# Performance work log

Measured on AMD Instinct MI355X. Metric: run time of the kernel, lower is better.

Reference implementation:

```python
import jax, jax.numpy as jnp
import numpy as np

L, D, V = 3, 512, 100        # num_layers, num_dimensions, vocabulary_size
B, S, SE = 128, 512, 512     # batch, decoder seq len, encoder seq len


def setup_inputs() -> dict:
    key = jax.random.key(0)
    ks = jax.random.split(key, 16)
    s = 1.0 / np.sqrt(D)
    u = lambda k, shape: jax.random.uniform(k, shape, jnp.float32, -s, s)
    return {
        "padded_seqs": jax.random.randint(ks[0], (B, S), 0, V),
        "seq_lengths": jax.random.randint(ks[1], (B,), 1, S + 1),
        "encoder_padded_seqs": jax.random.normal(ks[2], (B, SE, D), jnp.float32),
        "hidden_states": jax.random.normal(ks[3], (L, B, D), jnp.float32),
        "embedding": jax.random.normal(ks[4], (V, D), jnp.float32) * 0.02,
        "gru_w_ih": u(ks[5], (L, 3 * D, D)),
        "gru_w_hh": u(ks[6], (L, 3 * D, D)),
        "gru_b_ih": u(ks[7], (L, 3 * D)),
        "gru_b_hh": u(ks[8], (L, 3 * D)),
        "attn_w": u(ks[9], (D, 2 * D)),
        "attn_b": u(ks[10], (D,)),
        "out_w": u(ks[11], (V, D)),
        "out_b": u(ks[12], (V,)),
    }


def _gru(x, h0, w_ih, w_hh, b_ih, b_hh):
    """Multi-layer GRU, batch_first. x:(B,S,D), h0:(L,B,D). PyTorch gate order r,z,n."""
    h_finals = []
    for l in range(L):
        # precompute input projections for all timesteps: (B,S,3D)
        xp = jnp.einsum('bsd,ed->bse', x, w_ih[l]) + b_ih[l]
        whh, bhh = w_hh[l], b_hh[l]

        def step(h, xt):
            gh = h @ whh.T + bhh                      # (B,3D)
            xr, xz, xn = jnp.split(xt, 3, axis=-1)
            hr, hz, hn = jnp.split(gh, 3, axis=-1)
            r = jax.nn.sigmoid(xr + hr)
            z = jax.nn.sigmoid(xz + hz)
            n = jnp.tanh(xn + r * hn)
            h2 = (1.0 - z) * n + z * h
            return h2, h2

        hT, ys = jax.lax.scan(step, h0[l], jnp.swapaxes(xp, 0, 1))
        x = jnp.swapaxes(ys, 0, 1)                    # (B,S,D) output of this layer
        h_finals.append(hT)
    return x, jnp.stack(h_finals)


def reference(padded_seqs, seq_lengths, encoder_padded_seqs, hidden_states,
              embedding, gru_w_ih, gru_w_hh, gru_b_ih, gru_b_hh,
              attn_w, attn_b, out_w, out_b):
    # embedding (dropout=0 in eval)
    emb = embedding[padded_seqs]                      # (B,S,D)
    dec, h_out = _gru(emb, hidden_states, gru_w_ih, gru_w_hh, gru_b_ih, gru_b_hh)
    # mask from first hidden channel, exactly as the torch code
    mask = (dec[:, :, 0] != 0).astype(jnp.float32)[:, :, None]   # (B,S,1)
    # attention: scaled dot-product scores over encoder positions
    scores = jnp.einsum('bqd,bkd->bqk', dec, encoder_padded_seqs) / np.sqrt(D)
    attn_w8 = jax.nn.softmax(scores, axis=2)          # (B,S,SE)
    context = jnp.einsum('bqk,bkd->bqd', attn_w8, encoder_padded_seqs)
    cat = jnp.concatenate([dec, context], axis=2)     # (B,S,2D)
    attn_masked = jnp.tanh(cat @ attn_w.T + attn_b) * mask
    logits = (attn_masked @ out_w.T + out_b) * mask   # (B,S,V)
    return logits, h_out, attn_w8
```

## Files before the change

kernel.cpp:

```cpp
#include <hip/hip_runtime.h>


typedef unsigned short u16;
typedef __attribute__((ext_vector_type(8))) __bf16 bf16x8;
typedef __attribute__((ext_vector_type(4))) float f32x4;
typedef __attribute__((ext_vector_type(4))) unsigned int u32x4;

#define D_ 512
#define S_ 512
#define SE_ 512
#define B_ 128
#define V_ 100

__device__ __forceinline__ float bf2f(u16 v) {
  unsigned u = ((unsigned)v) << 16;
  return __builtin_bit_cast(float, u);
}
__device__ __forceinline__ u16 f2bf(float f) {
  unsigned u = __builtin_bit_cast(unsigned, f);
  u += 0x7FFF + ((u >> 16) & 1);
  return (u16)(u >> 16);
}

__global__ __launch_bounds__(256) void cvt_f32_bf16(const float* __restrict__ src,
                                                    u16* __restrict__ dst, long n4) {
  long i = (long)blockIdx.x * 256 + threadIdx.x;
  long stride = (long)gridDim.x * 256;
  for (; i < n4; i += stride) {
    float4 v = ((const float4*)src)[i];
    unsigned long long p = (unsigned long long)f2bf(v.x) |
                           ((unsigned long long)f2bf(v.y) << 16) |
                           ((unsigned long long)f2bf(v.z) << 32) |
                           ((unsigned long long)f2bf(v.w) << 48);
    ((unsigned long long*)dst)[i] = p;
  }
}

__global__ __launch_bounds__(256) void zero_flags(unsigned* __restrict__ f, int n) {
  int i = blockIdx.x * 256 + threadIdx.x;
  if (i < n)
    __hip_atomic_store(&f[i], 0u, __ATOMIC_RELAXED, __HIP_MEMORY_SCOPE_AGENT);
}

__global__ __launch_bounds__(256) void transpose_enc(const float* __restrict__ enc,
                                                     u16* __restrict__ encT) {
  __shared__ u16 tile[64][72];
  int b = blockIdx.z, d0 = blockIdx.x * 64, se0 = blockIdx.y * 64;
  const float* src = enc + (long)b * SE_ * D_;
  int t = threadIdx.x;
  int r = t >> 2, cq = (t & 3) * 16;
#pragma unroll
  for (int j = 0; j < 4; ++j) {
    float4 v = *(const float4*)(src + (long)(se0 + r) * D_ + d0 + cq + j * 4);
    tile[r][cq + j * 4 + 0] = f2bf(v.x);
    tile[r][cq + j * 4 + 1] = f2bf(v.y);
    tile[r][cq + j * 4 + 2] = f2bf(v.z);
    tile[r][cq + j * 4 + 3] = f2bf(v.w);
  }
  __syncthreads();
  u16* dst = encT + (long)b * D_ * SE_;
  u16 ov[16];
#pragma unroll
  for (int j = 0; j < 16; ++j) ov[j] = tile[cq + j][r];
  *(u32x4*)(dst + (long)(d0 + r) * SE_ + se0 + cq) = *(u32x4*)&ov[0];
  *(u32x4*)(dst + (long)(d0 + r) * SE_ + se0 + cq + 8) = *(u32x4*)&ov[8];
}

__global__ __launch_bounds__(256) void softmax_rows(float* __restrict__ sc,
                                                    u16* __restrict__ abf) {
  long row = (long)blockIdx.x * 4 + (threadIdx.x >> 6);
  int lane = threadIdx.x & 63;
  float* p = sc + row * 512;
  float4 v0 = ((const float4*)p)[lane * 2];
  float4 v1 = ((const float4*)p)[lane * 2 + 1];
  float vals[8] = {v0.x, v0.y, v0.z, v0.w, v1.x, v1.y, v1.z, v1.w};
  float m = vals[0];
#pragma unroll
  for (int j = 1; j < 8; ++j) m = fmaxf(m, vals[j]);
#pragma unroll
  for (int o = 32; o; o >>= 1) m = fmaxf(m, __shfl_xor(m, o, 64));
  float s = 0.f;
#pragma unroll
  for (int j = 0; j < 8; ++j) { vals[j] = __expf(vals[j] - m); s += vals[j]; }
#pragma unroll
  for (int o = 32; o; o >>= 1) s += __shfl_xor(s, o, 64);
  float inv = 1.f / s;
  u16 ob[8];
#pragma unroll
  for (int j = 0; j < 8; ++j) { vals[j] *= inv; ob[j] = f2bf(vals[j]); }
  float4 w0 = {vals[0], vals[1], vals[2], vals[3]};
  float4 w1 = {vals[4], vals[5], vals[6], vals[7]};
  ((float4*)p)[lane * 2] = w0;
  ((float4*)p)[lane * 2 + 1] = w1;
  *(u32x4*)(abf + row * 512 + lane * 8) = *(u32x4*)ob;
}

template <int MODE, int WF32>
__global__ __launch_bounds__(256) void gemm_xwt(
    const u16* __restrict__ A1, const u16* __restrict__ A2, const u16* __restrict__ W,
    const float* __restrict__ bias, void* __restrict__ Cout, const u16* __restrict__ maskSrc,
    int N, int K, int K1, long sAb, long sWb, long sCb, float scale, int ldc) {
  __shared__ u16 sA[128][32];
  __shared__ u16 sW_[128][32];
  int bz = blockIdx.z;
  int n0 = blockIdx.x * 128, m0 = blockIdx.y * 128;
  const u16* Ab = A1 + (long)bz * sAb;
  int t = threadIdx.x, wave = t >> 6, lane = t & 63;
  int wm = (wave >> 1) * 64, wn = (wave & 1) * 64;
  f32x4 acc[4][4] = {};
  for (int kk = 0; kk < K; kk += 32) {
#pragma unroll
    for (int i = 0; i < 2; ++i) {
      int id = t + i * 256;
      int row = id >> 2, c8 = (id & 3) * 8;
      const u16* src;
      if (MODE == 3 && kk >= K1)
        src = A2 + (long)(m0 + row) * (K - K1) + (kk - K1) + c8;
      else
        src = Ab + (long)(m0 + row) * K1 + kk + c8;
      *(u32x4*)&sA[row][c8] = *(const u32x4*)src;
    }
#pragma unroll
    for (int i = 0; i < 2; ++i) {
      int id = t + i * 256;
      int row = id >> 2, c8 = (id & 3) * 8;
      if (WF32) {
        const float* wsrc = ((const float*)W) + (long)bz * sWb + (long)(n0 + row) * K + kk + c8;
        float4 va = *(const float4*)wsrc;
        float4 vb = *(const float4*)(wsrc + 4);
        u16 tmp[8] = {f2bf(va.x), f2bf(va.y), f2bf(va.z), f2bf(va.w),
                      f2bf(vb.x), f2bf(vb.y), f2bf(vb.z), f2bf(vb.w)};
        *(u32x4*)&sW_[row][c8] = *(u32x4*)tmp;
      } else {
        u32x4 v = {0u, 0u, 0u, 0u};
        if (n0 + row < N) v = *(const u32x4*)(W + (long)bz * sWb + (long)(n0 + row) * K + kk + c8);
        *(u32x4*)&sW_[row][c8] = v;
      }
    }
    __syncthreads();
    int k8 = (lane >> 4) * 8, rr = lane & 15;
    bf16x8 wf[4];
#pragma unroll
    for (int nt = 0; nt < 4; ++nt)
      wf[nt] = __builtin_bit_cast(bf16x8, *(const u32x4*)&sW_[wn + nt * 16 + rr][k8]);
#pragma unroll
    for (int mt = 0; mt < 4; ++mt) {
      bf16x8 af = __builtin_bit_cast(bf16x8, *(const u32x4*)&sA[wm + mt * 16 + rr][k8]);
#pragma unroll
      for (int nt = 0; nt < 4; ++nt)
        acc[mt][nt] = __builtin_amdgcn_mfma_f32_16x16x32_bf16(af, wf[nt], acc[mt][nt], 0, 0, 0);
    }
    __syncthreads();
  }
  int rq = (lane >> 4) * 4, cl = lane & 15;
#pragma unroll
  for (int mt = 0; mt < 4; ++mt) {
#pragma unroll
    for (int nt = 0; nt < 4; ++nt) {
#pragma unroll
      for (int rg = 0; rg < 4; ++rg) {
        int row = m0 + wm + mt * 16 + rq + rg;
        int col = n0 + wn + nt * 16 + cl;
        float v = acc[mt][nt][rg];
        if (MODE == 1) {
          ((float*)Cout)[(long)bz * sCb + (long)row * ldc + col] = v * scale;
        } else if (MODE == 2) {
          ((u16*)Cout)[(long)bz * sCb + (long)row * ldc + col] = f2bf(v);
        } else if (MODE == 3) {
          float mk = (bf2f(maskSrc[(long)row * D_]) != 0.f) ? 1.f : 0.f;
          ((u16*)Cout)[(long)row * ldc + col] = f2bf(tanhf(v + bias[col]) * mk);
        } else {
          if (col < N) {
            float mk = (bf2f(maskSrc[(long)row * D_]) != 0.f) ? 1.f : 0.f;
            ((float*)Cout)[(long)row * ldc + col] = (v + bias[col]) * mk;
          }
        }
      }
    }
  }
}

__global__ __launch_bounds__(512, 1) void gru_wave(
    const int* __restrict__ tok, const float* __restrict__ embedding,
    const u16* __restrict__ wih_all, const u16* __restrict__ whh_all,
    const float* __restrict__ bih_all, const float* __restrict__ bhh_all,
    const float* __restrict__ hidden,
    unsigned* __restrict__ ring01, unsigned* __restrict__ ring2,
    unsigned* __restrict__ ringM1, unsigned* __restrict__ flags,
    u16* __restrict__ xout2, float* __restrict__ hfin) {
  __shared__ u16 sHA[32 * 512];
  __shared__ u16 sHB[32 * 512];
  __shared__ float sXP[2][32 * 101];
  __shared__ float sPART[24 * 272];
  const int bid = blockIdx.x;
  const int l = bid >> 6;
  const int bg = (bid >> 4) & 3;
  const int cg = bid & 15;
  const int tid = threadIdx.x;
  const int wave = tid >> 6;
  const bool isXp = wave >= 4;
  const int nh = (wave >> 1) & 1;
  const int kh = wave & 1;
  const int lane = tid & 63;
  const int rr = lane & 15, kq = lane >> 4;
  const int cl = rr, rq = kq;
  const int chL = nh * 16 + cl;
  const int ch = cg * 32 + chL;
  unsigned* myflags = flags + (l * 4 + bg) * 32 * 16;
  const unsigned* belowflags = (l > 0) ? flags + ((l - 1) * 4 + bg) * 32 * 16 : myflags;
  const u16* Wsrc = (isXp ? wih_all : whh_all) + (long)l * 786432;
  const float* bsrc = (isXp ? bih_all : bhh_all) + l * 1536;
  float bh[3];
#pragma unroll
  for (int g = 0; g < 3; ++g) bh[g] = bsrc[g * 512 + ch];

  auto ringAddr = [&](int lay, int t) -> unsigned* {
    if (t < 0) return ringM1 + lay * 32768;
    if (lay == 2) return ring2 + (long)t * 32768;
    return ring01 + ((long)lay * 512 + t) * 32768;
  };

  u32x4 wf[3][8];
#pragma unroll
  for (int g = 0; g < 3; ++g) {
    const u16* wrow =
        Wsrc + ((long)(g * 512 + cg * 32 + nh * 16 + rr)) * 512 + kh * 256 + kq * 8;
#pragma unroll
    for (int ks = 0; ks < 8; ++ks) wf[g][ks] = *(const u32x4*)(wrow + ks * 32);
  }

  float mh[2][4] = {};
  if (!isXp && kh == 0) {
#pragma unroll
    for (int mt = 0; mt < 2; ++mt)
#pragma unroll
      for (int rg = 0; rg < 4; ++rg)
        mh[mt][rg] =
            hidden[(long)l * 65536 + (long)(bg * 32 + mt * 16 + rq * 4 + rg) * 512 + ch];
  }

#pragma unroll 1
  for (int t = -1; t < S_; ++t) {
    const bool doXp = isXp && (t < S_ - 1);
#pragma unroll
    for (int g = 0; g < 3; ++g)
#pragma unroll
      for (int ks = 0; ks < 8; ++ks) asm volatile("" : "+v"(wf[g][ks]));

    if (doXp && l == 0) {
      int u = tid - 256;
#pragma unroll
      for (int i = 0; i < 2; ++i) {
        int task = u + i * 256;
        int row = task >> 4;
        int c0 = (task & 15) * 32;
        int tk = tok[(long)(bg * 32 + row) * 512 + (t + 1)];
        const float* es = embedding + (long)tk * 512 + c0;
        u16 tmp[32];
#pragma unroll
        for (int q = 0; q < 8; ++q) {
          float4 v = *(const float4*)(es + q * 4);
          tmp[q * 4 + 0] = f2bf(v.x); tmp[q * 4 + 1] = f2bf(v.y);
          tmp[q * 4 + 2] = f2bf(v.z); tmp[q * 4 + 3] = f2bf(v.w);
        }
#pragma unroll
        for (int q = 0; q < 4; ++q) {
          int grp = (c0 >> 3) + q;
          *(u32x4*)&sHB[row * 512 + ((grp ^ (row & 7)) * 8)] = *(u32x4*)&tmp[q * 8];
        }
      }
    }
    asm volatile("" ::: "memory");
    if (wave == 0) {
      const unsigned* fp = nullptr;
      int tgt = 0;
      if (lane < 32) { fp = myflags + lane * 16; tgt = t + 1; }
      else if (l > 0 && t < S_ - 1) { fp = belowflags + (lane - 32) * 16; tgt = t + 3; }
      int it = 0;
      bool ok;
      do {
        int v = fp ? (int)__hip_atomic_load(fp, __ATOMIC_RELAXED, __HIP_MEMORY_SCOPE_AGENT)
                   : 0x3fffffff;
        ok = (bool)__all(v >= tgt);
        if (!ok) __builtin_amdgcn_s_sleep(1);
      } while (!ok && ++it < (1 << 22));
    }
    __syncthreads();
    if (!isXp && t >= 0) {
      const unsigned* hsrc = ringAddr(l, t - 1) + bg * 32 * 256;
      u32x4 vv[8];
#pragma unroll
      for (int i = 0; i < 8; ++i) {
        int uu = tid + i * 256;
        const unsigned* src = hsrc + (uu >> 6) * 256 + (uu & 63) * 4;
        asm volatile("global_load_dwordx4 %0, %1, off sc0 sc1"
                     : "=&v"(vv[i]) : "v"(src) : "memory");
      }
      asm volatile("s_waitcnt vmcnt(0)" ::: "memory");
      __builtin_amdgcn_sched_barrier(0);
#pragma unroll
      for (int i = 0; i < 8; ++i) {
        int uu = tid + i * 256;
        int row = uu >> 6, c8 = uu & 63;
        *(u32x4*)&sHA[row * 512 + ((c8 ^ (row & 7)) * 8)] = vv[i];
      }
    } else if (doXp && l > 0) {
      const unsigned* hsrc = ringAddr(l - 1, t + 1) + bg * 32 * 256;
      u32x4 vv[8];
#pragma unroll
      for (int i = 0; i < 8; ++i) {
        int uu = (tid - 256) + i * 256;
        const unsigned* src = hsrc + (uu >> 6) * 256 + (uu & 63) * 4;
        asm volatile("global_load_dwordx4 %0, %1, off sc0 sc1"
                     : "=&v"(vv[i]) : "v"(src) : "memory");
      }
      asm volatile("s_waitcnt vmcnt(0)" ::: "memory");
      __builtin_amdgcn_sched_barrier(0);
#pragma unroll
      for (int i = 0; i < 8; ++i) {
        int uu = (tid - 256) + i * 256;
        int row = uu >> 6, c8 = uu & 63;
        *(u32x4*)&sHB[row * 512 + ((c8 ^ (row & 7)) * 8)] = vv[i];
      }
    }
    __syncthreads();
    f32x4 acc[2][3] = {};
    const bool doMM = isXp ? doXp : (t >= 0);
    if (doMM) {
      const u16* sH = isXp ? sHB : sHA;
#pragma unroll
      for (int mt = 0; mt < 2; ++mt) {
        const int abase = (mt * 16 + rr) * 512;
        const int axor = (mt * 16 + rr) & 7;
#pragma unroll
        for (int ks = 0; ks < 8; ++ks) {
          const int grp = kh * 32 + ks * 4 + kq;
          bf16x8 af = __builtin_bit_cast(
              bf16x8, *(const u32x4*)&sH[abase + ((grp ^ axor) * 8)]);
#pragma unroll
          for (int g = 0; g < 3; ++g)
            acc[mt][g] = __builtin_amdgcn_mfma_f32_16x16x32_bf16(
                af, __builtin_bit_cast(bf16x8, wf[g][ks]), acc[mt][g], 0, 0, 0);
        }
      }
      if (kh == 1) {
#pragma unroll
        for (int mt = 0; mt < 2; ++mt)
#pragma unroll
          for (int g = 0; g < 3; ++g) {
            float* sp = &sPART[((((isXp ? 2 : 0) + nh) * 2 + mt) * 3 + g) * 272];
#pragma unroll
            for (int rg = 0; rg < 4; ++rg)
              sp[(rq * 4 + rg) * 17 + cl] = acc[mt][g][rg];
          }
      }
    }
    __syncthreads();
    if (doMM && kh == 0) {
#pragma unroll
      for (int mt = 0; mt < 2; ++mt)
#pragma unroll
        for (int g = 0; g < 3; ++g) {
          const float* sp = &sPART[((((isXp ? 2 : 0) + nh) * 2 + mt) * 3 + g) * 272];
#pragma unroll
          for (int rg = 0; rg < 4; ++rg)
            acc[mt][g][rg] += sp[(rq * 4 + rg) * 17 + cl];
        }
      if (isXp) {
        float* xpd = sXP[(t + 1) & 1];
#pragma unroll
        for (int mt = 0; mt < 2; ++mt)
#pragma unroll
          for (int g = 0; g < 3; ++g)
#pragma unroll
            for (int rg = 0; rg < 4; ++rg)
              xpd[(mt * 16 + rq * 4 + rg) * 101 + g * 32 + chL] =
                  acc[mt][g][rg] + bh[g];
      }
    }
    if (!isXp && kh == 0) {
      const float* xps = sXP[t & 1];
      unsigned* rdst = ringAddr(l, t);
      unsigned xsv[2][4];
#pragma unroll
      for (int mt = 0; mt < 2; ++mt) {
        unsigned pk[4];
#pragma unroll
        for (int rg = 0; rg < 4; ++rg) {
          float h2;
          if (t >= 0) {
            int rloc = mt * 16 + rq * 4 + rg;
            float xr = xps[rloc * 101 + chL];
            float xz = xps[rloc * 101 + 32 + chL];
            float xn = xps[rloc * 101 + 64 + chL];
            float r = 1.f / (1.f + __expf(-(xr + acc[mt][0][rg] + bh[0])));
            float z = 1.f / (1.f + __expf(-(xz + acc[mt][1][rg] + bh[1])));
            float n = tanhf(xn + r * (acc[mt][2][rg] + bh[2]));
            h2 = (1.f - z) * n + z * mh[mt][rg];
            mh[mt][rg] = h2;
          } else {
            h2 = mh[mt][rg];
          }
          pk[rg] = (unsigned)f2bf(h2);
        }
        xsv[mt][0] = pk[0]; xsv[mt][1] = pk[1]; xsv[mt][2] = pk[2]; xsv[mt][3] = pk[3];
#pragma unroll
        for (int rg = 0; rg < 4; ++rg) {
          unsigned prt = (unsigned)__shfl_xor((int)pk[rg], 1);
          if (!(cl & 1))
            __hip_atomic_store(
                &rdst[(bg * 32 + mt * 16 + rq * 4 + rg) * 256 + (ch >> 1)],
                pk[rg] | (prt << 16), __ATOMIC_RELAXED, __HIP_MEMORY_SCOPE_AGENT);
        }
      }
      asm volatile("s_waitcnt vmcnt(0)" ::: "memory");
      if (lane == 0)
        __hip_atomic_store(&myflags[(cg * 2 + nh) * 16], (unsigned)(t + 2),
                           __ATOMIC_RELAXED, __HIP_MEMORY_SCOPE_AGENT);
      if (l == 2 && t >= 0) {
#pragma unroll
        for (int mt = 0; mt < 2; ++mt)
#pragma unroll
          for (int rg = 0; rg < 4; ++rg) {
            int rloc = mt * 16 + rq * 4 + rg;
            xout2[((long)(bg * 32 + rloc) * 512 + t) * 512 + ch] = (u16)xsv[mt][rg];
          }
      }
    }
  }
  if (!isXp && kh == 0) {
#pragma unroll
    for (int mt = 0; mt < 2; ++mt)
#pragma unroll
      for (int rg = 0; rg < 4; ++rg)
        hfin[(long)l * 65536 + (long)(bg * 32 + mt * 16 + rq * 4 + rg) * 512 + ch] =
            mh[mt][rg];
  }
}

extern "C" void kernel_launch(void* const* d_in, const int* in_sizes, int n_in,
                              void* d_out, int out_size, void* d_ws, size_t ws_size,
                              hipStream_t stream) {
  const int* padded    = (const int*)d_in[0];
  const float* enc     = (const float*)d_in[2];
  const float* hidden  = (const float*)d_in[3];
  const float* embedding = (const float*)d_in[4];
  const float* w_ih    = (const float*)d_in[5];
  const float* w_hh    = (const float*)d_in[6];
  const float* b_ih    = (const float*)d_in[7];
  const float* b_hh    = (const float*)d_in[8];
  const float* attn_w  = (const float*)d_in[9];
  const float* attn_b  = (const float*)d_in[10];
  const float* out_w   = (const float*)d_in[11];
  const float* out_b   = (const float*)d_in[12];

  if (ws_size < 280645632ULL) return;

  char* ws = (char*)d_ws;
  u16* W_IH   = (u16*)(ws + 0);
  u16* W_HH   = (u16*)(ws + 4718592);
  u16* ATTN_W = (u16*)(ws + 9437184);
  u16* OUT_W  = (u16*)(ws + 10485760);
  unsigned* FLAGS = (unsigned*)(ws + 10588160);
  unsigned* RINGM1 = (unsigned*)(ws + 10637312);
  u16* XA     = (u16*)(ws + 12210176);
  u16* XB     = (u16*)(ws + 79319040);
  u16* ENCT   = (u16*)(ws + 146427904);
  u16* AMASK  = (u16*)(ws + 213536768);
  u16* ATTN_BF = AMASK;

  float* out_logits = (float*)d_out;
  float* out_h      = out_logits + 6553600;
  float* out_attn   = out_h + 196608;

  unsigned* RING01 = (unsigned*)out_attn;
  unsigned* RING2  = (unsigned*)XA;

  zero_flags<<<24, 256, 0, stream>>>(FLAGS, 6144);
  cvt_f32_bf16<<<512, 256, 0, stream>>>(w_ih, W_IH, 2359296 / 4);
  cvt_f32_bf16<<<512, 256, 0, stream>>>(w_hh, W_HH, 2359296 / 4);
  cvt_f32_bf16<<<256, 256, 0, stream>>>(attn_w, ATTN_W, 524288 / 4);
  cvt_f32_bf16<<<64, 256, 0, stream>>>(out_w, OUT_W, 51200 / 4);
  transpose_enc<<<dim3(8, 8, 128), 256, 0, stream>>>(enc, ENCT);

  gru_wave<<<192, 512, 0, stream>>>(
      padded, embedding, W_IH, W_HH, b_ih, b_hh, hidden,
      RING01, RING2, RINGM1, FLAGS, XB, out_h);

  gemm_xwt<1, 1><<<dim3(4, 4, 128), 256, 0, stream>>>(
      XB, nullptr, (const u16*)enc, nullptr, out_attn, nullptr,
      512, 512, 512, 262144, 262144, 262144, 0.044194173824159216f, 512);
  softmax_rows<<<16384, 256, 0, stream>>>(out_attn, ATTN_BF);
  gemm_xwt<2, 0><<<dim3(4, 4, 128), 256, 0, stream>>>(
      ATTN_BF, nullptr, ENCT, nullptr, XA, nullptr,
      512, 512, 512, 262144, 262144, 262144, 1.f, 512);
  gemm_xwt<3, 0><<<dim3(4, 512, 1), 256, 0, stream>>>(
      XB, XA, ATTN_W, attn_b, AMASK, XB,
      512, 1024, 512, 0, 0, 0, 1.f, 512);
  gemm_xwt<4, 0><<<dim3(1, 512, 1), 256, 0, stream>>>(
      AMASK, nullptr, OUT_W, out_b, d_out, XB,
      100, 512, 512, 0, 0, 0, 1.f, 100);
}
```

Baseline: 3.340 ms.

## Deepen GRU input-projection pipeline to two steps ahead with triple-buffered sXP

The persistent wavefront GRU kernel now computes the input projection two timesteps ahead of the recurrent step instead of one. It uses a three-slot sXP buffer and shifts the flag targets and ring indices to match. The aim is more slack between layers, so a layer's x-projection for a future step does not wait on the layer below producing its output. The cost is one extra warm-up iteration, more shared memory, and a deeper wait on the below-layer flags. That deeper wait could lengthen the cross-layer critical path.

```diff
diff --git a/kernel.cpp b/kernel.cpp
--- a/kernel.cpp
+++ b/kernel.cpp
@@ -190,7 +190,7 @@
     u16* __restrict__ xout2, float* __restrict__ hfin) {
   __shared__ u16 sHA[32 * 512];
   __shared__ u16 sHB[32 * 512];
-  __shared__ float sXP[2][32 * 101];
+  __shared__ float sXP[3][32 * 101];
   __shared__ float sPART[24 * 272];
   const int bid = blockIdx.x;
   const int l = bid >> 6;
@@ -240,8 +240,9 @@
   }
 
 #pragma unroll 1
-  for (int t = -1; t < S_; ++t) {
-    const bool doXp = isXp && (t < S_ - 1);
+  for (int p = -2; p < S_; ++p) {
+    const bool doXp = isXp && (p <= S_ - 3);
+    const bool doGh = !isXp && (p >= 0);
 #pragma unroll
     for (int g = 0; g < 3; ++g)
 #pragma unroll
@@ -254,7 +255,7 @@
         int task = u + i * 256;
         int row = task >> 4;
         int c0 = (task & 15) * 32;
-        int tk = tok[(long)(bg * 32 + row) * 512 + (t + 1)];
+        int tk = tok[(long)(bg * 32 + row) * 512 + (p + 2)];
         const float* es = embedding + (long)tk * 512 + c0;
         u16 tmp[32];
 #pragma unroll
@@ -274,8 +275,8 @@
     if (wave == 0) {
       const unsigned* fp = nullptr;
       int tgt = 0;
-      if (lane < 32) { fp = myflags + lane * 16; tgt = t + 1; }
-      else if (l > 0 && t < S_ - 1) { fp = belowflags + (lane - 32) * 16; tgt = t + 3; }
+      if (lane < 32 && p >= 0) { fp = myflags + lane * 16; tgt = p + 2; }
+      else if (lane >= 32 && l > 0 && p <= S_ - 3) { fp = belowflags + (lane - 32) * 16; tgt = p + 5; }
       int it = 0;
       bool ok;
       do {
@@ -286,8 +287,8 @@
       } while (!ok && ++it < (1 << 22));
     }
     __syncthreads();
-    if (!isXp && t >= 0) {
-      const unsigned* hsrc = ringAddr(l, t - 1) + bg * 32 * 256;
+    if (doGh) {
+      const unsigned* hsrc = ringAddr(l, p - 1) + bg * 32 * 256;
       u32x4 vv[8];
 #pragma unroll
       for (int i = 0; i < 8; ++i) {
@@ -305,7 +306,7 @@
         *(u32x4*)&sHA[row * 512 + ((c8 ^ (row & 7)) * 8)] = vv[i];
       }
     } else if (doXp && l > 0) {
-      const unsigned* hsrc = ringAddr(l - 1, t + 1) + bg * 32 * 256;
+      const unsigned* hsrc = ringAddr(l - 1, p + 2) + bg * 32 * 256;
       u32x4 vv[8];
 #pragma unroll
       for (int i = 0; i < 8; ++i) {
@@ -325,7 +326,7 @@
     }
     __syncthreads();
     f32x4 acc[2][3] = {};
-    const bool doMM = isXp ? doXp : (t >= 0);
+    const bool doMM = isXp ? doXp : doGh;
     if (doMM) {
       const u16* sH = isXp ? sHB : sHA;
 #pragma unroll
@@ -367,7 +368,7 @@
             acc[mt][g][rg] += sp[(rq * 4 + rg) * 17 + cl];
         }
       if (isXp) {
-        float* xpd = sXP[(t + 1) & 1];
+        float* xpd = sXP[(p + 2) % 3];
 #pragma unroll
         for (int mt = 0; mt < 2; ++mt)
 #pragma unroll
@@ -378,9 +379,9 @@
                   acc[mt][g][rg] + bh[g];
       }
     }
-    if (!isXp && kh == 0) {
-      const float* xps = sXP[t & 1];
-      unsigned* rdst = ringAddr(l, t);
+    if (!isXp && kh == 0 && p >= -1) {
+      const float* xps = sXP[((p % 3) + 3) % 3];
+      unsigned* rdst = ringAddr(l, p);
       unsigned xsv[2][4];
 #pragma unroll
       for (int mt = 0; mt < 2; ++mt) {
@@ -388,7 +389,7 @@
 #pragma unroll
         for (int rg = 0; rg < 4; ++rg) {
           float h2;
-          if (t >= 0) {
+          if (p >= 0) {
             int rloc = mt * 16 + rq * 4 + rg;
             float xr = xps[rloc * 101 + chL];
             float xz = xps[rloc * 101 + 32 + chL];
@@ -415,15 +416,15 @@
       }
       asm volatile("s_waitcnt vmcnt(0)" ::: "memory");
       if (lane == 0)
-        __hip_atomic_store(&myflags[(cg * 2 + nh) * 16], (unsigned)(t + 2),
+        __hip_atomic_store(&myflags[(cg * 2 + nh) * 16], (unsigned)(p + 3),
                            __ATOMIC_RELAXED, __HIP_MEMORY_SCOPE_AGENT);
-      if (l == 2 && t >= 0) {
+      if (l == 2 && p >= 0) {
 #pragma unroll
         for (int mt = 0; mt < 2; ++mt)
 #pragma unroll
           for (int rg = 0; rg < 4; ++rg) {
             int rloc = mt * 16 + rq * 4 + rg;
-            xout2[((long)(bg * 32 + rloc) * 512 + t) * 512 + ch] = (u16)xsv[mt][rg];
+            xout2[((long)(bg * 32 + rloc) * 512 + p) * 512 + ch] = (u16)xsv[mt][rg];
           }
       }
     }
```

Result: slower. 3.462 ms (+3.7%).
